# Optimization experiments

Measured on AMD Instinct MI355X. Metric: run time of the kernel, lower is better.

The kernel has to match this reference:

```python
import jax, jax.numpy as jnp
import numpy as np

N_NODES = 100000
N_EDGES = 1600000
D_IN = 128
UNITS = 128


def setup_inputs() -> dict:
    key = jax.random.key(0)
    k1, k2, k3, k4, k5 = jax.random.split(key, 5)
    x = jax.random.normal(k1, (N_NODES, D_IN), dtype=jnp.float32)
    # glorot-uniform-like dense weight
    limit = float(np.sqrt(6.0 / (D_IN + UNITS)))
    w = jax.random.uniform(k2, (D_IN, UNITS), minval=-limit, maxval=limit, dtype=jnp.float32)
    # COO sparse adjacency: A[row, col] = val
    edge_row = jax.random.randint(k3, (N_EDGES,), 0, N_NODES, dtype=jnp.int32)
    edge_col = jax.random.randint(k4, (N_EDGES,), 0, N_NODES, dtype=jnp.int32)
    edge_val = jax.random.uniform(k5, (N_EDGES,), dtype=jnp.float32)
    return {"x": x, "w": w, "edge_row": edge_row, "edge_col": edge_col, "edge_val": edge_val}


def reference(x, w, edge_row, edge_col, edge_val):
    # dropout rate = 0.0 -> identity (module default)
    xw = x @ w                                   # [N, units] dense projection
    # sparse adjacency propagation: out[i] = sum_e val[e] * xw[col[e]] for row[e]==i
    msgs = xw[edge_col] * edge_val[:, None]      # [E, units] irregular gather
    out = jax.ops.segment_sum(msgs, edge_row, num_segments=x.shape[0])
    return jax.nn.relu(out)                      # activation
```

## Files before the change

kernel.cpp:

```cpp
#include <hip/hip_runtime.h>

#define N_NODES 100000
#define N_EDGES 1600000
#define D 128
#define NB 512
#define BCAP 3584
#define BSTRIDE 16
#define CHUNK 4000
#define NSCAT 400
#define NGEMMB 521
#define NTILES 1563
#define HCAP 1792
#define CTS 132

typedef __attribute__((ext_vector_type(8))) short  short8;
typedef __attribute__((ext_vector_type(4))) float  floatx4;

__device__ __forceinline__ ushort f2bf(float f) {
    unsigned u = __float_as_uint(f);
    u += 0x7FFF + ((u >> 16) & 1);
    return (ushort)(u >> 16);
}
__device__ __forceinline__ float bf2f(ushort s) {
    return __uint_as_float((unsigned)s << 16);
}
__device__ __forceinline__ int bucket_of(int r)  { return (int)(((unsigned)r << 9) / 100000u); }
__device__ __forceinline__ int row_start(int b)  { return (b * 100000 + 511) >> 9; }

union SMem {
    struct {
        int2  stage[CHUNK];
        int   sA[NB];
        int   sB[NB];
        int   lcur[NB];
        int   gbase[NB];
        short sbuck[CHUNK];
    } sc;
    struct {
        ushort wt[128 * 128];
        ushort ct[4][16 * CTS];
    } ge;
};

__global__ __launch_bounds__(256) void gemm_and_scatter(const float* __restrict__ x,
                                                        const float* __restrict__ w,
                                                        ushort* __restrict__ xwb,
                                                        const int* __restrict__ erow,
                                                        const int* __restrict__ ecol,
                                                        const float* __restrict__ eval,
                                                        int* __restrict__ bcnt,
                                                        int2* __restrict__ bkt) {
    __shared__ SMem sm;
    const int t = threadIdx.x;

    if (blockIdx.x < NGEMMB) {
        ushort* wt = sm.ge.wt;
        const int wv   = t >> 6;
        const int lane = t & 63;
        const int m    = lane & 15;
        const int q    = lane >> 4;

        {
            const float4* w4 = (const float4*)w;
            for (int i = t; i < 4096; i += 256) {
                const float4 v = w4[i];
                const int k = i >> 5;
                const int n = (i & 31) << 2;
                const int c = k >> 3, kc = k & 7;
#pragma unroll
                for (int d = 0; d < 4; ++d) {
                    const float val = (d == 0) ? v.x : (d == 1) ? v.y : (d == 2) ? v.z : v.w;
                    const int nn = n + d;
                    wt[(nn << 7) | (((c ^ (nn & 15)) & 15) << 3) | kc] = f2bf(val);
                }
            }
        }
        __syncthreads();

        float4 xa[8];
        {
            const int rb0 = blockIdx.x * 64 + wv * 16;
            const float* xr = x + (size_t)min(rb0 + m, N_NODES - 1) * D + q * 8;
#pragma unroll
            for (int k2 = 0; k2 < 4; ++k2) {
                xa[k2 * 2 + 0] = *(const float4*)(xr + k2 * 32);
                xa[k2 * 2 + 1] = *(const float4*)(xr + k2 * 32 + 4);
            }
        }

        for (int tb = blockIdx.x; tb < NTILES; tb += NGEMMB) {
            const int rbase = tb * 64 + wv * 16;

            short8 afr[4];
#pragma unroll
            for (int k2 = 0; k2 < 4; ++k2) {
                const float4 a0 = xa[k2 * 2 + 0];
                const float4 a1 = xa[k2 * 2 + 1];
                short8 a;
                a[0] = (short)f2bf(a0.x); a[1] = (short)f2bf(a0.y);
                a[2] = (short)f2bf(a0.z); a[3] = (short)f2bf(a0.w);
                a[4] = (short)f2bf(a1.x); a[5] = (short)f2bf(a1.y);
                a[6] = (short)f2bf(a1.z); a[7] = (short)f2bf(a1.w);
                afr[k2] = a;
            }

            const int tnext = tb + NGEMMB;
            if (tnext < NTILES) {
                const int rbn = tnext * 64 + wv * 16;
                const float* xr = x + (size_t)min(rbn + m, N_NODES - 1) * D + q * 8;
#pragma unroll
                for (int k2 = 0; k2 < 4; ++k2) {
                    xa[k2 * 2 + 0] = *(const float4*)(xr + k2 * 32);
                    xa[k2 * 2 + 1] = *(const float4*)(xr + k2 * 32 + 4);
                }
            }

            floatx4 acc[8];
#pragma unroll
            for (int tt = 0; tt < 8; ++tt) acc[tt] = (floatx4){0.f, 0.f, 0.f, 0.f};

#pragma unroll
            for (int k2 = 0; k2 < 4; ++k2) {
#pragma unroll
                for (int tt = 0; tt < 8; ++tt) {
                    const int n  = tt * 16 + m;
                    const int cc = (((k2 << 2) + q) ^ m) & 15;
                    const short8 b = *(const short8*)&wt[(n << 7) | (cc << 3)];
                    acc[tt] = __builtin_amdgcn_mfma_f32_16x16x32_bf16(afr[k2], b, acc[tt], 0, 0, 0);
                }
            }

#pragma unroll
            for (int tt = 0; tt < 8; ++tt) {
#pragma unroll
                for (int r = 0; r < 4; ++r) {
                    sm.ge.ct[wv][((q << 2) | r) * CTS + tt * 16 + m] = f2bf(acc[tt][r]);
                }
            }
            const int rl  = lane >> 2;
            const int ch  = lane & 3;
            const int row = rbase + rl;
            if (row < N_NODES) {
                const ushort* srcp = &sm.ge.ct[wv][rl * CTS + ch * 32];
                ushort*       dstp = &xwb[(size_t)row * D + ch * 32];
#pragma unroll
                for (int u = 0; u < 4; ++u) {
                    ((int4*)dstp)[u] = ((const int4*)srcp)[u];
                }
            }
        }
    } else {
        const int e0 = (blockIdx.x - NGEMMB) * CHUNK;
        int*   sA    = sm.sc.sA;
        int*   sB    = sm.sc.sB;
        int*   lcur  = sm.sc.lcur;
        int*   gbase = sm.sc.gbase;
        short* sbuck = sm.sc.sbuck;
        int2*  stage = sm.sc.stage;

        sA[t] = 0; sA[t + 256] = 0;
        __syncthreads();

        for (int i = t; i < CHUNK; i += 256) {
            atomicAdd(&sA[bucket_of(erow[e0 + i])], 1);
        }
        __syncthreads();

        int cur = 0;
        int* bufs[2] = {sA, sB};
#pragma unroll
        for (int o = 1; o < 512; o <<= 1) {
            const int* src = bufs[cur];
            int*       dst = bufs[cur ^ 1];
            const int i0 = t, i1 = t + 256;
            dst[i0] = src[i0] + ((i0 >= o) ? src[i0 - o] : 0);
            dst[i1] = src[i1] + ((i1 >= o) ? src[i1 - o] : 0);
            cur ^= 1;
            __syncthreads();
        }
        {
            const int* incl = bufs[cur];
            int*       excl = bufs[cur ^ 1];
            excl[t]       = (t == 0) ? 0 : incl[t - 1];
            excl[t + 256] = incl[t + 255];
        }
        __syncthreads();
        int* L = bufs[cur ^ 1];

        for (int b = t; b < NB; b += 256) {
            lcur[b] = L[b];
            const int cnt = ((b == NB - 1) ? CHUNK : L[b + 1]) - L[b];
            gbase[b] = (cnt > 0) ? atomicAdd(&bcnt[b * BSTRIDE], cnt) : 0;
        }
        __syncthreads();

        for (int i = t; i < CHUNK; i += 256) {
            const int   r = erow[e0 + i];
            const int   c = ecol[e0 + i];
            const float v = eval[e0 + i];
            const int   b = bucket_of(r);
            const int  rl = r - row_start(b);
            const int pos = atomicAdd(&lcur[b], 1);
            stage[pos] = make_int2((rl << 17) | c, __float_as_int(v));
            sbuck[pos] = (short)b;
        }
        __syncthreads();

        for (int i = t; i < CHUNK; i += 256) {
            const int b   = sbuck[i];
            const int dst = gbase[b] + (i - L[b]);
            if (dst < BCAP) bkt[(size_t)b * BCAP + dst] = stage[i];
        }
    }
}

__global__ __launch_bounds__(256, 4) void csr_gather(const int* __restrict__ bcnt,
                                                     const int2* __restrict__ bkt,
                                                     const ushort* __restrict__ xwb,
                                                     float* __restrict__ out) {
    __shared__ int2 lcsr[HCAP];
    __shared__ int  sA[256], sB[256], lcur[256];
    const int bg = blockIdx.x;
    const int b  = bg >> 1;
    const int h  = bg & 1;
    const int t  = threadIdx.x;
    const int n  = min(bcnt[b * BSTRIDE], BCAP);
    const int r0    = row_start(b);
    const int nrows = row_start(b + 1) - r0;
    const int mid   = (nrows + 1) >> 1;
    const int lo    = h ? mid : 0;
    const int hi    = h ? nrows : mid;
    const int nloc  = hi - lo;

    const int2* src = bkt + (size_t)b * BCAP;
    sA[t] = 0;
    __syncthreads();

    for (int i = t; i < n; i += 256) {
        const int rl = (int)(((unsigned)src[i].x) >> 17);
        if (rl >= lo && rl < hi) atomicAdd(&sA[rl - lo], 1);
    }
    __syncthreads();

    int cur = 0;
    int* bufs[2] = {sA, sB};
#pragma unroll
    for (int o = 1; o < 256; o <<= 1) {
        const int* s = bufs[cur];
        int*       d = bufs[cur ^ 1];
        d[t] = s[t] + ((t >= o) ? s[t - o] : 0);
        cur ^= 1;
        __syncthreads();
    }
    lcur[t] = (t == 0) ? 0 : bufs[cur][t - 1];
    __syncthreads();

    for (int i = t; i < n; i += 256) {
        const int2 e = src[i];
        const int rl = (int)(((unsigned)e.x) >> 17);
        if (rl >= lo && rl < hi) {
            const int pos = atomicAdd(&lcur[rl - lo], 1);
            if (pos < HCAP) lcsr[pos] = make_int2(e.x & 0x1FFFF, e.y);
        }
    }
    __syncthreads();

    const int qid = t >> 4;
    const int lc  = (t & 15) << 3;

    for (int ln = qid; ln < nloc; ln += 16) {
        int start = (ln == 0) ? 0 : lcur[ln - 1];
        int end   = lcur[ln];
        start = min(start, HCAP);
        end   = min(end, HCAP);

        float acc[8] = {0, 0, 0, 0, 0, 0, 0, 0};

        for (int j = start; j < end; j += 4) {
            const int jb = j + 1, jc = j + 2, jd = j + 3;
            const int2 e0 = lcsr[j];
            const int2 e1 = lcsr[min(jb, end - 1)];
            const int2 e2 = lcsr[min(jc, end - 1)];
            const int2 e3 = lcsr[min(jd, end - 1)];
            const short8 m0 = *(const short8*)&xwb[(size_t)e0.x * D + lc];
            const short8 m1 = *(const short8*)&xwb[(size_t)e1.x * D + lc];
            const short8 m2 = *(const short8*)&xwb[(size_t)e2.x * D + lc];
            const short8 m3 = *(const short8*)&xwb[(size_t)e3.x * D + lc];
            const float v0 = __int_as_float(e0.y);
            const float v1 = (jb < end) ? __int_as_float(e1.y) : 0.f;
            const float v2 = (jc < end) ? __int_as_float(e2.y) : 0.f;
            const float v3 = (jd < end) ? __int_as_float(e3.y) : 0.f;
#pragma unroll
            for (int i = 0; i < 8; ++i) {
                acc[i] += v0 * bf2f((ushort)m0[i]);
                acc[i] += v1 * bf2f((ushort)m1[i]);
                acc[i] += v2 * bf2f((ushort)m2[i]);
                acc[i] += v3 * bf2f((ushort)m3[i]);
            }
        }

        float* o = out + (size_t)(r0 + lo + ln) * D + lc;
        *(float4*)(o + 0) = make_float4(fmaxf(acc[0], 0.f), fmaxf(acc[1], 0.f),
                                        fmaxf(acc[2], 0.f), fmaxf(acc[3], 0.f));
        *(float4*)(o + 4) = make_float4(fmaxf(acc[4], 0.f), fmaxf(acc[5], 0.f),
                                        fmaxf(acc[6], 0.f), fmaxf(acc[7], 0.f));
    }
}

extern "C" void kernel_launch(void* const* d_in, const int* in_sizes, int n_in,
                              void* d_out, int out_size, void* d_ws, size_t ws_size,
                              hipStream_t stream) {
    const float* x    = (const float*)d_in[0];
    const float* w    = (const float*)d_in[1];
    const int*   erow = (const int*)d_in[2];
    const int*   ecol = (const int*)d_in[3];
    const float* eval = (const float*)d_in[4];
    float*       out  = (float*)d_out;

    char*   ws_base = (char*)d_ws;
    ushort* xwb  = (ushort*)ws_base;
    int*    bcnt = (int*)(ws_base + 25600000);
    int2*   bkt  = (int2*)(ws_base + 25632768);

    (void)hipMemsetAsync(bcnt, 0, 32768, stream);

    gemm_and_scatter<<<NGEMMB + NSCAT, 256, 0, stream>>>(x, w, xwb, erow, ecol, eval, bcnt, bkt);
    csr_gather<<<NB * 2, 256, 0, stream>>>(bcnt, bkt, xwb, out);
}
```

Baseline: 215.9 us.

## Shrink GEMM staging LDS, reorder scatter blocks first, and rebalance edge chunks

The GEMM epilogue now stages the output tile in two halves with an XOR-swizzled 64-wide buffer instead of a padded 132-wide one. This shrinks the shared-memory footprint of the GEMM path and avoids bank conflicts. Scatter blocks now take the low block indices so they are dispatched first, and edges are split into 500 chunks of 3200 instead of 400 of 4000. A launch-bounds minimum of 4 blocks per CU is also added, which may force register limits or spills in the MFMA path.

```diff
diff --git a/kernel.cpp b/kernel.cpp
--- a/kernel.cpp
+++ b/kernel.cpp
@@ -6,12 +6,11 @@
 #define NB 512
 #define BCAP 3584
 #define BSTRIDE 16
-#define CHUNK 4000
-#define NSCAT 400
+#define CHUNK 3200
+#define NSCAT 500
 #define NGEMMB 521
 #define NTILES 1563
 #define HCAP 1792
-#define CTS 132
 
 typedef __attribute__((ext_vector_type(8))) short  short8;
 typedef __attribute__((ext_vector_type(4))) float  floatx4;
@@ -38,22 +37,23 @@
     } sc;
     struct {
         ushort wt[128 * 128];
-        ushort ct[4][16 * CTS];
+        ushort ct[4][16 * 64];
     } ge;
 };
 
-__global__ __launch_bounds__(256) void gemm_and_scatter(const float* __restrict__ x,
-                                                        const float* __restrict__ w,
-                                                        ushort* __restrict__ xwb,
-                                                        const int* __restrict__ erow,
-                                                        const int* __restrict__ ecol,
-                                                        const float* __restrict__ eval,
-                                                        int* __restrict__ bcnt,
-                                                        int2* __restrict__ bkt) {
+__global__ __launch_bounds__(256, 4) void gemm_and_scatter(const float* __restrict__ x,
+                                                           const float* __restrict__ w,
+                                                           ushort* __restrict__ xwb,
+                                                           const int* __restrict__ erow,
+                                                           const int* __restrict__ ecol,
+                                                           const float* __restrict__ eval,
+                                                           int* __restrict__ bcnt,
+                                                           int2* __restrict__ bkt) {
     __shared__ SMem sm;
     const int t = threadIdx.x;
 
-    if (blockIdx.x < NGEMMB) {
+    if (blockIdx.x >= NSCAT) {
+        const int bid  = blockIdx.x - NSCAT;
         ushort* wt = sm.ge.wt;
         const int wv   = t >> 6;
         const int lane = t & 63;
@@ -79,7 +79,7 @@
 
         float4 xa[8];
         {
-            const int rb0 = blockIdx.x * 64 + wv * 16;
+            const int rb0 = bid * 64 + wv * 16;
             const float* xr = x + (size_t)min(rb0 + m, N_NODES - 1) * D + q * 8;
 #pragma unroll
             for (int k2 = 0; k2 < 4; ++k2) {
@@ -88,7 +88,7 @@
             }
         }
 
-        for (int tb = blockIdx.x; tb < NTILES; tb += NGEMMB) {
+        for (int tb = bid; tb < NTILES; tb += NGEMMB) {
             const int rbase = tb * 64 + wv * 16;
 
             short8 afr[4];
@@ -131,26 +131,29 @@
             }
 
 #pragma unroll
-            for (int tt = 0; tt < 8; ++tt) {
-#pragma unroll
-                for (int r = 0; r < 4; ++r) {
-                    sm.ge.ct[wv][((q << 2) | r) * CTS + tt * 16 + m] = f2bf(acc[tt][r]);
-                }
-            }
-            const int rl  = lane >> 2;
-            const int ch  = lane & 3;
-            const int row = rbase + rl;
-            if (row < N_NODES) {
-                const ushort* srcp = &sm.ge.ct[wv][rl * CTS + ch * 32];
-                ushort*       dstp = &xwb[(size_t)row * D + ch * 32];
-#pragma unroll
-                for (int u = 0; u < 4; ++u) {
-                    ((int4*)dstp)[u] = ((const int4*)srcp)[u];
+            for (int p = 0; p < 2; ++p) {
+#pragma unroll
+                for (int tt2 = 0; tt2 < 4; ++tt2) {
+#pragma unroll
+                    for (int r = 0; r < 4; ++r) {
+                        const int row  = (q << 2) | r;
+                        const int slot = (tt2 ^ r ^ q) & 3;
+                        sm.ge.ct[wv][row * 64 + slot * 16 + m] = f2bf(acc[p * 4 + tt2][r]);
+                    }
+                }
+                const int rl   = lane >> 2;
+                const int ch   = lane & 3;
+                const int slot = (ch ^ (rl & 3) ^ (rl >> 2)) & 3;
+                const ushort* srcp = &sm.ge.ct[wv][rl * 64 + slot * 16];
+                if (rbase + rl < N_NODES) {
+                    ushort* dstp = &xwb[(size_t)(rbase + rl) * D + p * 64 + ch * 16];
+                    ((int4*)dstp)[0] = ((const int4*)srcp)[0];
+                    ((int4*)dstp)[1] = ((const int4*)srcp)[1];
                 }
             }
         }
     } else {
-        const int e0 = (blockIdx.x - NGEMMB) * CHUNK;
+        const int e0 = blockIdx.x * CHUNK;
         int*   sA    = sm.sc.sA;
         int*   sB    = sm.sc.sB;
         int*   lcur  = sm.sc.lcur;
@@ -324,6 +327,6 @@
 
     (void)hipMemsetAsync(bcnt, 0, 32768, stream);
 
-    gemm_and_scatter<<<NGEMMB + NSCAT, 256, 0, stream>>>(x, w, xwb, erow, ecol, eval, bcnt, bkt);
+    gemm_and_scatter<<<NSCAT + NGEMMB, 256, 0, stream>>>(x, w, xwb, erow, ecol, eval, bcnt, bkt);
     csr_gather<<<NB * 2, 256, 0, stream>>>(bcnt, bkt, xwb, out);
 }
```

Result: no change. 214.1 us (-0.8%).
